# Optimization experiments

Measured on AMD Instinct MI355X. Metric: run time of the kernel, lower is better.

Reference implementation:

```python
import jax, jax.numpy as jnp
import numpy as np

B, T, EMB, HS = 4, 4096, 1024, 64
BASE = 10000.0


def rope_angles(T, hs, base=BASE):
    # theta_i = base^(-2i/hs), freqs[t, i] = t * theta_i  -> (T, hs//2)
    inv = 1.0 / (base ** (2.0 * jnp.arange(hs // 2, dtype=jnp.float32) / hs))
    return jnp.arange(T, dtype=jnp.float32)[:, None] * inv[None, :]


def apply_rope(x, cos, sin):
    # x: (B, T, D); pairs are interleaved (even, odd) like torch.view_as_complex
    xr = x.reshape(*x.shape[:-1], -1, 2)
    xe, xo = xr[..., 0], xr[..., 1]
    re = xe * cos - xo * sin
    im = xe * sin + xo * cos
    return jnp.stack([re, im], axis=-1).reshape(x.shape)


def setup_inputs() -> dict:
    key = jax.random.key(0)
    kx, kq, kk, kv = jax.random.split(key, 4)
    s = 1.0 / np.sqrt(EMB)
    return {
        "x": jax.random.normal(kx, (B, T, EMB), jnp.float32),
        "Wq": jax.random.normal(kq, (HS, EMB), jnp.float32) * s,
        "Wk": jax.random.normal(kk, (HS, EMB), jnp.float32) * s,
        "Wv": jax.random.normal(kv, (HS, EMB), jnp.float32) * s,
    }


def reference(x, Wq, Wk, Wv):
    Tlen = x.shape[1]
    ang = rope_angles(Tlen, HS)          # (T, HS//2)
    cos, sin = jnp.cos(ang), jnp.sin(ang)
    q = x @ Wq.T                          # (B, T, HS)
    k = x @ Wk.T
    v = x @ Wv.T
    q = apply_rope(q, cos, sin)
    k = apply_rope(k, cos, sin)
    scores = jnp.einsum("bqd,bkd->bqk", q, k) * (HS ** -0.5)
    causal = jnp.tril(jnp.ones((Tlen, Tlen), dtype=bool))
    scores = jnp.where(causal[None], scores, -jnp.inf)
    w = jax.nn.softmax(scores, axis=-1)   # dropout in eval mode: identity
    return jnp.einsum("bqk,bkd->bqd", w, v)
```

## Files before the change

kernel.cpp:

```cpp
#include <hip/hip_runtime.h>

typedef __bf16 bf16x8 __attribute__((ext_vector_type(8)));
typedef __bf16 bf16x4 __attribute__((ext_vector_type(4)));
typedef float f32x4 __attribute__((ext_vector_type(4)));
typedef float f32x16 __attribute__((ext_vector_type(16)));
typedef unsigned int u32;

#define T_LEN 4096

__device__ __forceinline__ f32x4 mfma16(bf16x8 a, bf16x8 b, f32x4 c) {
    return __builtin_amdgcn_mfma_f32_16x16x32_bf16(a, b, c, 0, 0, 0);
}
__device__ __forceinline__ f32x16 mfma32(bf16x8 a, bf16x8 b, f32x16 c) {
    return __builtin_amdgcn_mfma_f32_32x32x16_bf16(a, b, c, 0, 0, 0);
}
__device__ __forceinline__ u32 packbf(float lo, float hi) {
    union { __bf16 e[2]; u32 w; } u;
    u.e[0] = (__bf16)lo; u.e[1] = (__bf16)hi;
    return u.w;
}
__device__ __forceinline__ f32x16 zero16() {
    f32x16 z;
    #pragma unroll
    for (int i = 0; i < 16; i++) z[i] = 0.f;
    return z;
}

__global__ __launch_bounds__(256) void convert_w_kernel(
    const float* __restrict__ Wq, const float* __restrict__ Wk,
    const float* __restrict__ Wv, __bf16* __restrict__ wb)
{
    int i = blockIdx.x * 256 + threadIdx.x;
    int m = i >> 14, off = (i & 16383) << 2;
    const float* s = (m == 0 ? Wq : (m == 1 ? Wk : Wv)) + off;
    float4 f = *(const float4*)s;
    bf16x4 h = { (__bf16)f.x, (__bf16)f.y, (__bf16)f.z, (__bf16)f.w };
    *(bf16x4*)(wb + (m << 16) + off) = h;
}

__global__ __launch_bounds__(256) void proj_kernel(
    const float* __restrict__ x, const __bf16* __restrict__ wb,
    __bf16* __restrict__ qb, __bf16* __restrict__ kb, __bf16* __restrict__ vt)
{
    __shared__ __bf16 xs[2][32][72];
    __shared__ __bf16 wl[2][192][72];
    const int tid  = threadIdx.x;
    const int wave = tid >> 6, lane = tid & 63;
    const int l15 = lane & 15, l4 = lane >> 4;
    const size_t m0 = (size_t)blockIdx.x * 32;
    const int xrow = tid >> 3, xcp = (tid & 7) * 8;
    const int wrow = tid >> 3, wcp = (tid & 7) * 8;

    f32x4 acc[2][3];
    #pragma unroll
    for (int a = 0; a < 2; a++)
        #pragma unroll
        for (int bn = 0; bn < 3; bn++) acc[a][bn] = (f32x4){0.f, 0.f, 0.f, 0.f};

    const float* xsrc = x + (m0 + xrow) * 1024 + xcp;

    float4 rx0, rx1;
    bf16x8 rw[6];

    rx0 = *(const float4*)(xsrc);
    rx1 = *(const float4*)(xsrc + 4);
    #pragma unroll
    for (int j = 0; j < 6; j++)
        rw[j] = *(const bf16x8*)(wb + (size_t)(wrow + j * 32) * 1024 + wcp);
    {
        bf16x8 h = {(__bf16)rx0.x, (__bf16)rx0.y, (__bf16)rx0.z, (__bf16)rx0.w,
                    (__bf16)rx1.x, (__bf16)rx1.y, (__bf16)rx1.z, (__bf16)rx1.w};
        *(bf16x8*)&xs[0][xrow][xcp] = h;
        #pragma unroll
        for (int j = 0; j < 6; j++)
            *(bf16x8*)&wl[0][wrow + j * 32][wcp] = rw[j];
    }
    __syncthreads();

    for (int t = 0; t < 16; t++) {
        const int cur = t & 1;
        if (t < 15) {
            const int k0 = (t + 1) * 64;
            rx0 = *(const float4*)(xsrc + k0);
            rx1 = *(const float4*)(xsrc + k0 + 4);
            #pragma unroll
            for (int j = 0; j < 6; j++)
                rw[j] = *(const bf16x8*)(wb + (size_t)(wrow + j * 32) * 1024 + k0 + wcp);
        }
        bf16x8 af[2][2], bfr[3][2];
        #pragma unroll
        for (int mf = 0; mf < 2; mf++)
            #pragma unroll
            for (int c = 0; c < 2; c++)
                af[mf][c] = *(const bf16x8*)&xs[cur][mf * 16 + l15][c * 32 + l4 * 8];
        #pragma unroll
        for (int nf = 0; nf < 3; nf++)
            #pragma unroll
            for (int c = 0; c < 2; c++)
                bfr[nf][c] = *(const bf16x8*)&wl[cur][wave * 48 + nf * 16 + l15][c * 32 + l4 * 8];
        #pragma unroll
        for (int mf = 0; mf < 2; mf++)
            #pragma unroll
            for (int nf = 0; nf < 3; nf++)
                #pragma unroll
                for (int c = 0; c < 2; c++)
                    acc[mf][nf] = mfma16(af[mf][c], bfr[nf][c], acc[mf][nf]);
        if (t < 15) {
            bf16x8 h = {(__bf16)rx0.x, (__bf16)rx0.y, (__bf16)rx0.z, (__bf16)rx0.w,
                        (__bf16)rx1.x, (__bf16)rx1.y, (__bf16)rx1.z, (__bf16)rx1.w};
            *(bf16x8*)&xs[cur ^ 1][xrow][xcp] = h;
            #pragma unroll
            for (int j = 0; j < 6; j++)
                *(bf16x8*)&wl[cur ^ 1][wrow + j * 32][wcp] = rw[j];
        }
        __syncthreads();
    }

    #pragma unroll
    for (int mf = 0; mf < 2; mf++) {
        #pragma unroll
        for (int nf = 0; nf < 3; nf++) {
            int n = wave * 48 + nf * 16 + l15;
            #pragma unroll
            for (int r = 0; r < 4; r++) {
                size_t mrow = m0 + mf * 16 + l4 * 4 + r;
                float val = acc[mf][nf][r];
                float partner = __shfl_xor(val, 1);
                if (n < 128) {
                    int i = (n & 63) >> 1;
                    int t = (int)(mrow & 4095);
                    float inv = __builtin_exp2f((float)i * (-13.287712379549449f / 32.f));
                    float ang = (float)t * inv;
                    float sn, cs;
                    __sincosf(ang, &sn, &cs);
                    float res = (n & 1) ? (partner * sn + val * cs)
                                        : (val * cs - partner * sn);
                    if (n < 64) {
                        res *= 0.180336884f;
                        qb[mrow * 64 + n] = (__bf16)res;
                    } else {
                        kb[mrow * 64 + (n - 64)] = (__bf16)res;
                    }
                } else {
                    int bb = (int)(mrow >> 12), tt = (int)(mrow & 4095);
                    vt[((size_t)bb * 64 + (n - 128)) * 4096 + tt] = (__bf16)val;
                }
            }
        }
    }
}

__global__ __launch_bounds__(512, 2) void flash_kernel(
    const __bf16* __restrict__ qb, const __bf16* __restrict__ kb,
    const __bf16* __restrict__ vt, float* __restrict__ out)
{
    __shared__ float ods[8][32][68];
    __shared__ float mls[2][8][32];

    const int tid = threadIdx.x;
    const int wave = tid >> 6, lane = tid & 63;
    const int l31 = lane & 31, h = lane >> 5;
    const int b = blockIdx.x & 3;
    const int p = blockIdx.x >> 2;
    const int prow = ((l31 >> 3) & 1) * 16 + ((l31 >> 2) & 1) * 8
                   + (l31 >> 4) * 4 + (l31 & 3);

    const __bf16* kbb = kb + (size_t)b * T_LEN * 64;
    const __bf16* vtb = vt + (size_t)b * 64 * T_LEN;

    #pragma unroll 1
    for (int half = 0; half < 2; half++) {
        const int jt = half ? p : 127 - p;
        const int q0 = jt * 32;
        const int qg = q0 + l31;

        const __bf16* qp = qb + ((size_t)b * T_LEN + q0 + l31) * 64 + h * 8;
        bf16x8 qf[4];
        #pragma unroll
        for (int dc = 0; dc < 4; dc++) qf[dc] = *(const bf16x8*)(qp + dc * 16);

        float m = -1e30f, l = 0.f;
        f32x16 o0 = zero16(), o1 = zero16();
        const int nt = (jt >> 1) + 1;

        for (int kt = wave; kt < nt; kt += 8) {
            const int kc0 = kt << 6;
            const __bf16* kr0 = kbb + (size_t)(kc0 + prow) * 64 + h * 8;
            const __bf16* kr1 = kr0 + 32 * 64;
            f32x16 s0 = zero16(), s1 = zero16();
            #pragma unroll
            for (int dc = 0; dc < 4; dc++) {
                s0 = mfma32(*(const bf16x8*)(kr0 + dc * 16), qf[dc], s0);
                s1 = mfma32(*(const bf16x8*)(kr1 + dc * 16), qf[dc], s1);
            }
            const __bf16* vr0 = vtb + (size_t)l31 * T_LEN + kc0 + h * 8;
            const __bf16* vr1 = vr0 + (size_t)32 * T_LEN;
            bf16x8 vf0[4], vf1[4];
            #pragma unroll
            for (int cg = 0; cg < 4; cg++) {
                vf0[cg] = *(const bf16x8*)(vr0 + cg * 16);
                vf1[cg] = *(const bf16x8*)(vr1 + cg * 16);
            }
            if (kc0 + 63 > q0) {
                #pragma unroll
                for (int r = 0; r < 16; r++) {
                    int koff = kc0 + ((r >> 2) & 1) * 16 + 8 * h
                             + (r >> 3) * 4 + (r & 3);
                    if (koff > qg)      s0[r] = -1e30f;
                    if (koff + 32 > qg) s1[r] = -1e30f;
                }
            }
            float tmax = -1e30f;
            #pragma unroll
            for (int r = 0; r < 16; r++) tmax = fmaxf(tmax, fmaxf(s0[r], s1[r]));
            tmax = fmaxf(tmax, __shfl_xor(tmax, 32));
            if (!__all(tmax <= m + 8.f)) {
                const float mnew = fmaxf(m, tmax);
                const float alpha = __builtin_exp2f(m - mnew);
                m = mnew;
                l *= alpha;
                #pragma unroll
                for (int r = 0; r < 16; r++) { o0[r] *= alpha; o1[r] *= alpha; }
            }
            float tsum = 0.f;
            #pragma unroll
            for (int r = 0; r < 16; r++) {
                float e0 = __builtin_exp2f(s0[r] - m);
                float e1 = __builtin_exp2f(s1[r] - m);
                s0[r] = e0; s1[r] = e1;
                tsum += e0 + e1;
            }
            tsum += __shfl_xor(tsum, 32);
            l += tsum;
            union { u32 w[4]; bf16x8 v; } pf[4];
            #pragma unroll
            for (int cg = 0; cg < 2; cg++) {
                pf[cg].w[0]     = packbf(s0[4 * cg + 0],  s0[4 * cg + 1]);
                pf[cg].w[1]     = packbf(s0[4 * cg + 2],  s0[4 * cg + 3]);
                pf[cg].w[2]     = packbf(s0[4 * cg + 8],  s0[4 * cg + 9]);
                pf[cg].w[3]     = packbf(s0[4 * cg + 10], s0[4 * cg + 11]);
                pf[cg + 2].w[0] = packbf(s1[4 * cg + 0],  s1[4 * cg + 1]);
                pf[cg + 2].w[1] = packbf(s1[4 * cg + 2],  s1[4 * cg + 3]);
                pf[cg + 2].w[2] = packbf(s1[4 * cg + 8],  s1[4 * cg + 9]);
                pf[cg + 2].w[3] = packbf(s1[4 * cg + 10], s1[4 * cg + 11]);
            }
            #pragma unroll
            for (int cg = 0; cg < 4; cg++) {
                o0 = mfma32(vf0[cg], pf[cg].v, o0);
                o1 = mfma32(vf1[cg], pf[cg].v, o1);
            }
        }

        #pragma unroll
        for (int c2 = 0; c2 < 4; c2++) {
            f32x4 w0 = {o0[4 * c2], o0[4 * c2 + 1], o0[4 * c2 + 2], o0[4 * c2 + 3]};
            f32x4 w1 = {o1[4 * c2], o1[4 * c2 + 1], o1[4 * c2 + 2], o1[4 * c2 + 3]};
            *(f32x4*)&ods[wave][l31][8 * c2 + 4 * h]      = w0;
            *(f32x4*)&ods[wave][l31][32 + 8 * c2 + 4 * h] = w1;
        }
        if (h == 0) { mls[0][wave][l31] = m; mls[1][wave][l31] = l; }
        __syncthreads();

        {
            const int q = tid >> 4, dc = tid & 15;
            float M = -1e30f;
            #pragma unroll
            for (int s2 = 0; s2 < 8; s2++) M = fmaxf(M, mls[0][s2][q]);
            float w8[8], L = 0.f;
            #pragma unroll
            for (int s2 = 0; s2 < 8; s2++) {
                float ws = __builtin_exp2f(mls[0][s2][q] - M);
                w8[s2] = ws;
                L += ws * mls[1][s2][q];
            }
            const float invL = 1.f / L;
            f32x4 acc = {0.f, 0.f, 0.f, 0.f};
            #pragma unroll
            for (int s2 = 0; s2 < 8; s2++) {
                f32x4 part = *(const f32x4*)&ods[s2][q][dc * 4];
                acc.x += part.x * w8[s2];
                acc.y += part.y * w8[s2];
                acc.z += part.z * w8[s2];
                acc.w += part.w * w8[s2];
            }
            acc.x *= invL; acc.y *= invL; acc.z *= invL; acc.w *= invL;
            *(f32x4*)(out + ((size_t)b * T_LEN + q0 + q) * 64 + dc * 4) = acc;
        }
        __syncthreads();
    }
}

extern "C" void kernel_launch(void* const* d_in, const int* in_sizes, int n_in,
                              void* d_out, int out_size, void* d_ws, size_t ws_size,
                              hipStream_t stream)
{
    const float* x  = (const float*)d_in[0];
    const float* Wq = (const float*)d_in[1];
    const float* Wk = (const float*)d_in[2];
    const float* Wv = (const float*)d_in[3];
    float* out = (float*)d_out;

    __bf16* qb = (__bf16*)d_ws;
    __bf16* kb = qb + 1048576;
    __bf16* vt = kb + 1048576;
    __bf16* wb = vt + 1048576;

    convert_w_kernel<<<192, 256, 0, stream>>>(Wq, Wk, Wv, wb);
    proj_kernel<<<512, 256, 0, stream>>>(x, wb, qb, kb, vt);
    flash_kernel<<<256, 512, 0, stream>>>(qb, kb, vt, out);
}
```

Baseline: 66.30 us.

## Retile projection to 64-row blocks and give each flash block one query tile

The projection kernel now uses 512-thread blocks that cover 64 rows of x, with 8 waves in a 2x4 grid, so each W tile in LDS is reused across twice as many rows. The flash kernel drops the paired long/short query-tile loop: each of 512 blocks handles one 32-row query tile, and the occupancy hint rises to 4 blocks per CU. The max and sum reductions are split into tree and partial accumulators to shorten dependency chains. The aim is more parallelism and better latency hiding, at the cost of losing the per-block causal work balancing and putting more register pressure on the flash kernel.

```diff
diff --git a/kernel.cpp b/kernel.cpp
--- a/kernel.cpp
+++ b/kernel.cpp
@@ -38,18 +38,18 @@
     *(bf16x4*)(wb + (m << 16) + off) = h;
 }
 
-__global__ __launch_bounds__(256) void proj_kernel(
+__global__ __launch_bounds__(512, 4) void proj_kernel(
     const float* __restrict__ x, const __bf16* __restrict__ wb,
     __bf16* __restrict__ qb, __bf16* __restrict__ kb, __bf16* __restrict__ vt)
 {
-    __shared__ __bf16 xs[2][32][72];
+    __shared__ __bf16 xs[2][64][72];
     __shared__ __bf16 wl[2][192][72];
     const int tid  = threadIdx.x;
     const int wave = tid >> 6, lane = tid & 63;
     const int l15 = lane & 15, l4 = lane >> 4;
-    const size_t m0 = (size_t)blockIdx.x * 32;
-    const int xrow = tid >> 3, xcp = (tid & 7) * 8;
-    const int wrow = tid >> 3, wcp = (tid & 7) * 8;
+    const int wm = wave >> 2, wn = wave & 3;
+    const size_t m0 = (size_t)blockIdx.x * 64;
+    const int srow = tid >> 3, scp = (tid & 7) * 8;
 
     f32x4 acc[2][3];
     #pragma unroll
@@ -57,23 +57,23 @@
         #pragma unroll
         for (int bn = 0; bn < 3; bn++) acc[a][bn] = (f32x4){0.f, 0.f, 0.f, 0.f};
 
-    const float* xsrc = x + (m0 + xrow) * 1024 + xcp;
+    const float* xsrc = x + (m0 + srow) * 1024 + scp;
 
     float4 rx0, rx1;
-    bf16x8 rw[6];
+    bf16x8 rw[3];
 
     rx0 = *(const float4*)(xsrc);
     rx1 = *(const float4*)(xsrc + 4);
     #pragma unroll
-    for (int j = 0; j < 6; j++)
-        rw[j] = *(const bf16x8*)(wb + (size_t)(wrow + j * 32) * 1024 + wcp);
+    for (int j = 0; j < 3; j++)
+        rw[j] = *(const bf16x8*)(wb + (size_t)(srow + j * 64) * 1024 + scp);
     {
         bf16x8 h = {(__bf16)rx0.x, (__bf16)rx0.y, (__bf16)rx0.z, (__bf16)rx0.w,
                     (__bf16)rx1.x, (__bf16)rx1.y, (__bf16)rx1.z, (__bf16)rx1.w};
-        *(bf16x8*)&xs[0][xrow][xcp] = h;
-        #pragma unroll
-        for (int j = 0; j < 6; j++)
-            *(bf16x8*)&wl[0][wrow + j * 32][wcp] = rw[j];
+        *(bf16x8*)&xs[0][srow][scp] = h;
+        #pragma unroll
+        for (int j = 0; j < 3; j++)
+            *(bf16x8*)&wl[0][srow + j * 64][scp] = rw[j];
     }
     __syncthreads();
 
@@ -84,20 +84,20 @@
             rx0 = *(const float4*)(xsrc + k0);
             rx1 = *(const float4*)(xsrc + k0 + 4);
             #pragma unroll
-            for (int j = 0; j < 6; j++)
-                rw[j] = *(const bf16x8*)(wb + (size_t)(wrow + j * 32) * 1024 + k0 + wcp);
+            for (int j = 0; j < 3; j++)
+                rw[j] = *(const bf16x8*)(wb + (size_t)(srow + j * 64) * 1024 + k0 + scp);
         }
         bf16x8 af[2][2], bfr[3][2];
         #pragma unroll
         for (int mf = 0; mf < 2; mf++)
             #pragma unroll
             for (int c = 0; c < 2; c++)
-                af[mf][c] = *(const bf16x8*)&xs[cur][mf * 16 + l15][c * 32 + l4 * 8];
+                af[mf][c] = *(const bf16x8*)&xs[cur][wm * 32 + mf * 16 + l15][c * 32 + l4 * 8];
         #pragma unroll
         for (int nf = 0; nf < 3; nf++)
             #pragma unroll
             for (int c = 0; c < 2; c++)
-                bfr[nf][c] = *(const bf16x8*)&wl[cur][wave * 48 + nf * 16 + l15][c * 32 + l4 * 8];
+                bfr[nf][c] = *(const bf16x8*)&wl[cur][wn * 48 + nf * 16 + l15][c * 32 + l4 * 8];
         #pragma unroll
         for (int mf = 0; mf < 2; mf++)
             #pragma unroll
@@ -108,10 +108,10 @@
         if (t < 15) {
             bf16x8 h = {(__bf16)rx0.x, (__bf16)rx0.y, (__bf16)rx0.z, (__bf16)rx0.w,
                         (__bf16)rx1.x, (__bf16)rx1.y, (__bf16)rx1.z, (__bf16)rx1.w};
-            *(bf16x8*)&xs[cur ^ 1][xrow][xcp] = h;
-            #pragma unroll
-            for (int j = 0; j < 6; j++)
-                *(bf16x8*)&wl[cur ^ 1][wrow + j * 32][wcp] = rw[j];
+            *(bf16x8*)&xs[cur ^ 1][srow][scp] = h;
+            #pragma unroll
+            for (int j = 0; j < 3; j++)
+                *(bf16x8*)&wl[cur ^ 1][srow + j * 64][scp] = rw[j];
         }
         __syncthreads();
     }
@@ -120,10 +120,10 @@
     for (int mf = 0; mf < 2; mf++) {
         #pragma unroll
         for (int nf = 0; nf < 3; nf++) {
-            int n = wave * 48 + nf * 16 + l15;
+            int n = wn * 48 + nf * 16 + l15;
             #pragma unroll
             for (int r = 0; r < 4; r++) {
-                size_t mrow = m0 + mf * 16 + l4 * 4 + r;
+                size_t mrow = m0 + wm * 32 + mf * 16 + l4 * 4 + r;
                 float val = acc[mf][nf][r];
                 float partner = __shfl_xor(val, 1);
                 if (n < 128) {
@@ -150,7 +150,7 @@
     }
 }
 
-__global__ __launch_bounds__(512, 2) void flash_kernel(
+__global__ __launch_bounds__(512, 4) void flash_kernel(
     const __bf16* __restrict__ qb, const __bf16* __restrict__ kb,
     const __bf16* __restrict__ vt, float* __restrict__ out)
 {
@@ -161,132 +161,132 @@
     const int wave = tid >> 6, lane = tid & 63;
     const int l31 = lane & 31, h = lane >> 5;
     const int b = blockIdx.x & 3;
-    const int p = blockIdx.x >> 2;
+    const int jt = 127 - (blockIdx.x >> 2);
+    const int q0 = jt * 32;
+    const int qg = q0 + l31;
     const int prow = ((l31 >> 3) & 1) * 16 + ((l31 >> 2) & 1) * 8
                    + (l31 >> 4) * 4 + (l31 & 3);
 
     const __bf16* kbb = kb + (size_t)b * T_LEN * 64;
     const __bf16* vtb = vt + (size_t)b * 64 * T_LEN;
 
-    #pragma unroll 1
-    for (int half = 0; half < 2; half++) {
-        const int jt = half ? p : 127 - p;
-        const int q0 = jt * 32;
-        const int qg = q0 + l31;
-
-        const __bf16* qp = qb + ((size_t)b * T_LEN + q0 + l31) * 64 + h * 8;
-        bf16x8 qf[4];
-        #pragma unroll
-        for (int dc = 0; dc < 4; dc++) qf[dc] = *(const bf16x8*)(qp + dc * 16);
-
-        float m = -1e30f, l = 0.f;
-        f32x16 o0 = zero16(), o1 = zero16();
-        const int nt = (jt >> 1) + 1;
-
-        for (int kt = wave; kt < nt; kt += 8) {
-            const int kc0 = kt << 6;
-            const __bf16* kr0 = kbb + (size_t)(kc0 + prow) * 64 + h * 8;
-            const __bf16* kr1 = kr0 + 32 * 64;
-            f32x16 s0 = zero16(), s1 = zero16();
-            #pragma unroll
-            for (int dc = 0; dc < 4; dc++) {
-                s0 = mfma32(*(const bf16x8*)(kr0 + dc * 16), qf[dc], s0);
-                s1 = mfma32(*(const bf16x8*)(kr1 + dc * 16), qf[dc], s1);
+    const __bf16* qp = qb + ((size_t)b * T_LEN + q0 + l31) * 64 + h * 8;
+    bf16x8 qf[4];
+    #pragma unroll
+    for (int dc = 0; dc < 4; dc++) qf[dc] = *(const bf16x8*)(qp + dc * 16);
+
+    float m = -1e30f, l = 0.f;
+    f32x16 o0 = zero16(), o1 = zero16();
+    const int nt = (jt >> 1) + 1;
+
+    for (int kt = wave; kt < nt; kt += 8) {
+        const int kc0 = kt << 6;
+        const __bf16* kr0 = kbb + (size_t)(kc0 + prow) * 64 + h * 8;
+        const __bf16* kr1 = kr0 + 32 * 64;
+        f32x16 s0 = zero16(), s1 = zero16();
+        #pragma unroll
+        for (int dc = 0; dc < 4; dc++) {
+            s0 = mfma32(*(const bf16x8*)(kr0 + dc * 16), qf[dc], s0);
+            s1 = mfma32(*(const bf16x8*)(kr1 + dc * 16), qf[dc], s1);
+        }
+        const __bf16* vr0 = vtb + (size_t)l31 * T_LEN + kc0 + h * 8;
+        const __bf16* vr1 = vr0 + (size_t)32 * T_LEN;
+        bf16x8 vf0[4], vf1[4];
+        #pragma unroll
+        for (int cg = 0; cg < 4; cg++) {
+            vf0[cg] = *(const bf16x8*)(vr0 + cg * 16);
+            vf1[cg] = *(const bf16x8*)(vr1 + cg * 16);
+        }
+        if (kc0 + 63 > q0) {
+            #pragma unroll
+            for (int r = 0; r < 16; r++) {
+                int koff = kc0 + ((r >> 2) & 1) * 16 + 8 * h
+                         + (r >> 3) * 4 + (r & 3);
+                if (koff > qg)      s0[r] = -1e30f;
+                if (koff + 32 > qg) s1[r] = -1e30f;
             }
-            const __bf16* vr0 = vtb + (size_t)l31 * T_LEN + kc0 + h * 8;
-            const __bf16* vr1 = vr0 + (size_t)32 * T_LEN;
-            bf16x8 vf0[4], vf1[4];
-            #pragma unroll
-            for (int cg = 0; cg < 4; cg++) {
-                vf0[cg] = *(const bf16x8*)(vr0 + cg * 16);
-                vf1[cg] = *(const bf16x8*)(vr1 + cg * 16);
-            }
-            if (kc0 + 63 > q0) {
-                #pragma unroll
-                for (int r = 0; r < 16; r++) {
-                    int koff = kc0 + ((r >> 2) & 1) * 16 + 8 * h
-                             + (r >> 3) * 4 + (r & 3);
-                    if (koff > qg)      s0[r] = -1e30f;
-                    if (koff + 32 > qg) s1[r] = -1e30f;
-                }
-            }
-            float tmax = -1e30f;
-            #pragma unroll
-            for (int r = 0; r < 16; r++) tmax = fmaxf(tmax, fmaxf(s0[r], s1[r]));
-            tmax = fmaxf(tmax, __shfl_xor(tmax, 32));
-            if (!__all(tmax <= m + 8.f)) {
-                const float mnew = fmaxf(m, tmax);
-                const float alpha = __builtin_exp2f(m - mnew);
-                m = mnew;
-                l *= alpha;
-                #pragma unroll
-                for (int r = 0; r < 16; r++) { o0[r] *= alpha; o1[r] *= alpha; }
-            }
-            float tsum = 0.f;
-            #pragma unroll
-            for (int r = 0; r < 16; r++) {
-                float e0 = __builtin_exp2f(s0[r] - m);
-                float e1 = __builtin_exp2f(s1[r] - m);
-                s0[r] = e0; s1[r] = e1;
-                tsum += e0 + e1;
-            }
-            tsum += __shfl_xor(tsum, 32);
-            l += tsum;
-            union { u32 w[4]; bf16x8 v; } pf[4];
-            #pragma unroll
-            for (int cg = 0; cg < 2; cg++) {
-                pf[cg].w[0]     = packbf(s0[4 * cg + 0],  s0[4 * cg + 1]);
-                pf[cg].w[1]     = packbf(s0[4 * cg + 2],  s0[4 * cg + 3]);
-                pf[cg].w[2]     = packbf(s0[4 * cg + 8],  s0[4 * cg + 9]);
-                pf[cg].w[3]     = packbf(s0[4 * cg + 10], s0[4 * cg + 11]);
-                pf[cg + 2].w[0] = packbf(s1[4 * cg + 0],  s1[4 * cg + 1]);
-                pf[cg + 2].w[1] = packbf(s1[4 * cg + 2],  s1[4 * cg + 3]);
-                pf[cg + 2].w[2] = packbf(s1[4 * cg + 8],  s1[4 * cg + 9]);
-                pf[cg + 2].w[3] = packbf(s1[4 * cg + 10], s1[4 * cg + 11]);
-            }
-            #pragma unroll
-            for (int cg = 0; cg < 4; cg++) {
-                o0 = mfma32(vf0[cg], pf[cg].v, o0);
-                o1 = mfma32(vf1[cg], pf[cg].v, o1);
-            }
-        }
-
-        #pragma unroll
-        for (int c2 = 0; c2 < 4; c2++) {
-            f32x4 w0 = {o0[4 * c2], o0[4 * c2 + 1], o0[4 * c2 + 2], o0[4 * c2 + 3]};
-            f32x4 w1 = {o1[4 * c2], o1[4 * c2 + 1], o1[4 * c2 + 2], o1[4 * c2 + 3]};
-            *(f32x4*)&ods[wave][l31][8 * c2 + 4 * h]      = w0;
-            *(f32x4*)&ods[wave][l31][32 + 8 * c2 + 4 * h] = w1;
-        }
-        if (h == 0) { mls[0][wave][l31] = m; mls[1][wave][l31] = l; }
-        __syncthreads();
-
-        {
-            const int q = tid >> 4, dc = tid & 15;
-            float M = -1e30f;
-            #pragma unroll
-            for (int s2 = 0; s2 < 8; s2++) M = fmaxf(M, mls[0][s2][q]);
-            float w8[8], L = 0.f;
-            #pragma unroll
-            for (int s2 = 0; s2 < 8; s2++) {
-                float ws = __builtin_exp2f(mls[0][s2][q] - M);
-                w8[s2] = ws;
-                L += ws * mls[1][s2][q];
-            }
-            const float invL = 1.f / L;
-            f32x4 acc = {0.f, 0.f, 0.f, 0.f};
-            #pragma unroll
-            for (int s2 = 0; s2 < 8; s2++) {
-                f32x4 part = *(const f32x4*)&ods[s2][q][dc * 4];
-                acc.x += part.x * w8[s2];
-                acc.y += part.y * w8[s2];
-                acc.z += part.z * w8[s2];
-                acc.w += part.w * w8[s2];
-            }
-            acc.x *= invL; acc.y *= invL; acc.z *= invL; acc.w *= invL;
-            *(f32x4*)(out + ((size_t)b * T_LEN + q0 + q) * 64 + dc * 4) = acc;
-        }
-        __syncthreads();
+        }
+        float tm[8];
+        #pragma unroll
+        for (int i = 0; i < 8; i++)
+            tm[i] = fmaxf(fmaxf(s0[2 * i], s0[2 * i + 1]),
+                          fmaxf(s1[2 * i], s1[2 * i + 1]));
+        #pragma unroll
+        for (int i = 0; i < 4; i++) tm[i] = fmaxf(tm[i], tm[i + 4]);
+        float tmax = fmaxf(fmaxf(tm[0], tm[1]), fmaxf(tm[2], tm[3]));
+        tmax = fmaxf(tmax, __shfl_xor(tmax, 32));
+        if (!__all(tmax <= m + 8.f)) {
+            const float mnew = fmaxf(m, tmax);
+            const float alpha = __builtin_exp2f(m - mnew);
+            m = mnew;
+            l *= alpha;
+            #pragma unroll
+            for (int r = 0; r < 16; r++) { o0[r] *= alpha; o1[r] *= alpha; }
+        }
+        float ts[4] = {0.f, 0.f, 0.f, 0.f};
+        #pragma unroll
+        for (int r = 0; r < 16; r++) {
+            float e0 = __builtin_exp2f(s0[r] - m);
+            float e1 = __builtin_exp2f(s1[r] - m);
+            s0[r] = e0; s1[r] = e1;
+            ts[r & 3] += e0 + e1;
+        }
+        float tsum = (ts[0] + ts[1]) + (ts[2] + ts[3]);
+        tsum += __shfl_xor(tsum, 32);
+        l += tsum;
+        union { u32 w[4]; bf16x8 v; } pf[4];
+        #pragma unroll
+        for (int cg = 0; cg < 2; cg++) {
+            pf[cg].w[0]     = packbf(s0[4 * cg + 0],  s0[4 * cg + 1]);
+            pf[cg].w[1]     = packbf(s0[4 * cg + 2],  s0[4 * cg + 3]);
+            pf[cg].w[2]     = packbf(s0[4 * cg + 8],  s0[4 * cg + 9]);
+            pf[cg].w[3]     = packbf(s0[4 * cg + 10], s0[4 * cg + 11]);
+            pf[cg + 2].w[0] = packbf(s1[4 * cg + 0],  s1[4 * cg + 1]);
+            pf[cg + 2].w[1] = packbf(s1[4 * cg + 2],  s1[4 * cg + 3]);
+            pf[cg + 2].w[2] = packbf(s1[4 * cg + 8],  s1[4 * cg + 9]);
+            pf[cg + 2].w[3] = packbf(s1[4 * cg + 10], s1[4 * cg + 11]);
+        }
+        #pragma unroll
+        for (int cg = 0; cg < 4; cg++) {
+            o0 = mfma32(vf0[cg], pf[cg].v, o0);
+            o1 = mfma32(vf1[cg], pf[cg].v, o1);
+        }
+    }
+
+    #pragma unroll
+    for (int c2 = 0; c2 < 4; c2++) {
+        f32x4 w0 = {o0[4 * c2], o0[4 * c2 + 1], o0[4 * c2 + 2], o0[4 * c2 + 3]};
+        f32x4 w1 = {o1[4 * c2], o1[4 * c2 + 1], o1[4 * c2 + 2], o1[4 * c2 + 3]};
+        *(f32x4*)&ods[wave][l31][8 * c2 + 4 * h]      = w0;
+        *(f32x4*)&ods[wave][l31][32 + 8 * c2 + 4 * h] = w1;
+    }
+    if (h == 0) { mls[0][wave][l31] = m; mls[1][wave][l31] = l; }
+    __syncthreads();
+
+    {
+        const int q = tid >> 4, dc = tid & 15;
+        float M = -1e30f;
+        #pragma unroll
+        for (int s2 = 0; s2 < 8; s2++) M = fmaxf(M, mls[0][s2][q]);
+        float w8[8], L = 0.f;
+        #pragma unroll
+        for (int s2 = 0; s2 < 8; s2++) {
+            float ws = __builtin_exp2f(mls[0][s2][q] - M);
+            w8[s2] = ws;
+            L += ws * mls[1][s2][q];
+        }
+        const float invL = 1.f / L;
+        f32x4 acc = {0.f, 0.f, 0.f, 0.f};
+        #pragma unroll
+        for (int s2 = 0; s2 < 8; s2++) {
+            f32x4 part = *(const f32x4*)&ods[s2][q][dc * 4];
+            acc.x += part.x * w8[s2];
+            acc.y += part.y * w8[s2];
+            acc.z += part.z * w8[s2];
+            acc.w += part.w * w8[s2];
+        }
+        acc.x *= invL; acc.y *= invL; acc.z *= invL; acc.w *= invL;
+        *(f32x4*)(out + ((size_t)b * T_LEN + q0 + q) * 64 + dc * 4) = acc;
     }
 }
 
@@ -306,6 +306,6 @@
     __bf16* wb = vt + 1048576;
 
     convert_w_kernel<<<192, 256, 0, stream>>>(Wq, Wk, Wv, wb);
-    proj_kernel<<<512, 256, 0, stream>>>(x, wb, qb, kb, vt);
-    flash_kernel<<<256, 512, 0, stream>>>(qb, kb, vt, out);
-}
+    proj_kernel<<<256, 512, 0, stream>>>(x, wb, qb, kb, vt);
+    flash_kernel<<<512, 512, 0, stream>>>(qb, kb, vt, out);
+}
```

After: 86.51 us. 30.5% more time.
